# Optimization experiments

Hardware: AMD Instinct MI355X
Metric: run time of the kernel (lower is better)

## Reference

```python
import jax, jax.numpy as jnp
import numpy as np

H = 1024        # hidden_dim
NH = 8          # num_heads
HD = H // NH    # head_dim
EPS = 1e-5


def setup_inputs() -> dict:
    key = jax.random.key(0)
    ks = jax.random.split(key, 16)
    s = 0.02
    d = {
        'x': jax.random.normal(ks[0], (2, 2048, H), dtype=jnp.float32),
        'ln1_g': jnp.ones((H,), jnp.float32), 'ln1_b': jnp.zeros((H,), jnp.float32),
        'ln2_g': jnp.ones((H,), jnp.float32), 'ln2_b': jnp.zeros((H,), jnp.float32),
        'Wq': jax.random.normal(ks[1], (H, H), jnp.float32) * s,
        'bq': jnp.zeros((H,), jnp.float32),
        'Wk': jax.random.normal(ks[2], (H, H), jnp.float32) * s,
        'bk': jnp.zeros((H,), jnp.float32),
        'Wv': jax.random.normal(ks[3], (H, H), jnp.float32) * s,
        'bv': jnp.zeros((H,), jnp.float32),
        'Wo': jax.random.normal(ks[4], (H, H), jnp.float32) * s,
        'bo': jnp.zeros((H,), jnp.float32),
        'W1': jax.random.normal(ks[5], (H, 4 * H), jnp.float32) * s,
        'b1': jnp.zeros((4 * H,), jnp.float32),
        'W2': jax.random.normal(ks[6], (4 * H, H), jnp.float32) * s,
        'b2': jnp.zeros((H,), jnp.float32),
    }
    return d


def _layernorm(x, g, b):
    mu = jnp.mean(x, axis=-1, keepdims=True)
    var = jnp.mean(jnp.square(x - mu), axis=-1, keepdims=True)
    return (x - mu) * jax.lax.rsqrt(var + EPS) * g + b


def _block(x, ln1_g, ln1_b, ln2_g, ln2_b, Wq, bq, Wk, bk, Wv, bv, Wo, bo, W1, b1, W2, b2):
    B, S, _ = x.shape
    h = _layernorm(x, ln1_g, ln1_b)
    q = (h @ Wq + bq).reshape(B, S, NH, HD).transpose(0, 2, 1, 3)  # [B,NH,S,HD]
    k = (h @ Wk + bk).reshape(B, S, NH, HD).transpose(0, 2, 1, 3)
    v = (h @ Wv + bv).reshape(B, S, NH, HD).transpose(0, 2, 1, 3)
    scores = jnp.einsum('bhqd,bhkd->bhqk', q, k) / np.sqrt(HD)
    causal = jnp.tril(jnp.ones((S, S), bool))
    scores = jnp.where(causal, scores, -jnp.inf)
    attn = jax.nn.softmax(scores, axis=-1)
    y = jnp.einsum('bhqk,bhkd->bhqd', attn, v).transpose(0, 2, 1, 3).reshape(B, S, H)
    x = x + y @ Wo + bo
    h2 = _layernorm(x, ln2_g, ln2_b)
    m = jax.nn.gelu(h2 @ W1 + b1, approximate=False) @ W2 + b2
    return x + m


def reference(x, ln1_g, ln1_b, ln2_g, ln2_b, Wq, bq, Wk, bk, Wv, bv, Wo, bo, W1, b1, W2, b2):
    return _block(x, ln1_g, ln1_b, ln2_g, ln2_b, Wq, bq, Wk, bk, Wv, bv, Wo, bo, W1, b1, W2, b2)
```

## Files before the change

kernel.cpp:

```cpp
#include <hip/hip_runtime.h>
#include <hip/hip_bf16.h>
#include <math.h>

using bf16 = __hip_bfloat16;
typedef __attribute__((ext_vector_type(8))) short short8v;
typedef __attribute__((ext_vector_type(4))) float f32x4;
typedef __attribute__((ext_vector_type(16))) float f32x16;

#define DEV __device__ __forceinline__

DEV void load_lds16(const bf16* gsrc, bf16* ldst) {
  __builtin_amdgcn_global_load_lds((const __attribute__((address_space(1))) void*)gsrc,
                                   (__attribute__((address_space(3))) void*)ldst, 16, 0, 0);
}

DEV void swz8(int& bx, int& by, int gx, int gy) {
  const int n = gx * gy, c = n >> 3;
  int lin = bx + gx * by;
  lin = (lin & 7) * c + (lin >> 3);
  bx = lin % gx; by = lin / gx;
}

DEV unsigned pack2bf(float a, float b) {
  bf16 ba = __float2bfloat16(a), bb = __float2bfloat16(b);
  return (unsigned)*(unsigned short*)&ba | ((unsigned)*(unsigned short*)&bb << 16);
}

__global__ __launch_bounds__(256) void prep_kernel(
    const float* __restrict__ Wq, const float* __restrict__ Wk, const float* __restrict__ Wv,
    const float* __restrict__ Wo, const float* __restrict__ W1, const float* __restrict__ W2,
    bf16* __restrict__ WqT, bf16* __restrict__ WkT, bf16* __restrict__ WvT,
    bf16* __restrict__ WoT, bf16* __restrict__ W1T, bf16* __restrict__ W2T,
    const float* __restrict__ x, const float* __restrict__ ln1g, const float* __restrict__ ln1b,
    bf16* __restrict__ h) {
  __shared__ float tile[64][65];
  const int b = blockIdx.x;
  if (b >= 3072) {
    const int row = b - 3072, t = threadIdx.x;
    const float4 v = ((const float4*)(x + (size_t)row * 1024))[t];
    float s = v.x + v.y + v.z + v.w;
#pragma unroll
    for (int mm = 1; mm < 64; mm <<= 1) s += __shfl_xor(s, mm);
    __shared__ float r1[4], r2[4];
    if ((t & 63) == 0) r1[t >> 6] = s;
    __syncthreads();
    const float mean = (r1[0] + r1[1] + r1[2] + r1[3]) * (1.0f / 1024.0f);
    const float d0 = v.x - mean, d1 = v.y - mean, d2 = v.z - mean, d3 = v.w - mean;
    float s2 = d0 * d0 + d1 * d1 + d2 * d2 + d3 * d3;
#pragma unroll
    for (int mm = 1; mm < 64; mm <<= 1) s2 += __shfl_xor(s2, mm);
    if ((t & 63) == 0) r2[t >> 6] = s2;
    __syncthreads();
    const float var = (r2[0] + r2[1] + r2[2] + r2[3]) * (1.0f / 1024.0f);
    const float rinv = rsqrtf(var + 1e-5f);
    const int c = t * 4;
    bf16* o = h + (size_t)row * 1024 + c;
    o[0] = __float2bfloat16(d0 * rinv * ln1g[c + 0] + ln1b[c + 0]);
    o[1] = __float2bfloat16(d1 * rinv * ln1g[c + 1] + ln1b[c + 1]);
    o[2] = __float2bfloat16(d2 * rinv * ln1g[c + 2] + ln1b[c + 2]);
    o[3] = __float2bfloat16(d3 * rinv * ln1g[c + 3] + ln1b[c + 3]);
    return;
  }
  const float* W; bf16* WT; int K, N, n0, k0;
  if (b < 1024) {
    const int which = b >> 8, t = b & 255;
    W  = (which == 0) ? Wq  : (which == 1) ? Wk  : (which == 2) ? Wv  : Wo;
    WT = (which == 0) ? WqT : (which == 1) ? WkT : (which == 2) ? WvT : WoT;
    K = 1024; N = 1024; n0 = (t & 15) * 64; k0 = (t >> 4) * 64;
  } else if (b < 2048) {
    const int t = b - 1024;
    W = W1; WT = W1T; K = 1024; N = 4096; n0 = (t & 63) * 64; k0 = (t >> 6) * 64;
  } else {
    const int t = b - 2048;
    W = W2; WT = W2T; K = 4096; N = 1024; n0 = (t & 15) * 64; k0 = (t >> 4) * 64;
  }
  const int tx = threadIdx.x & 15, ty = threadIdx.x >> 4;
#pragma unroll
  for (int p = 0; p < 4; ++p) {
    int r = p * 16 + ty;
    float4 vv = *(const float4*)&W[(size_t)(k0 + r) * N + n0 + tx * 4];
    tile[r][tx * 4 + 0] = vv.x; tile[r][tx * 4 + 1] = vv.y;
    tile[r][tx * 4 + 2] = vv.z; tile[r][tx * 4 + 3] = vv.w;
  }
  __syncthreads();
#pragma unroll
  for (int p = 0; p < 4; ++p) {
    int n = p * 16 + ty;
    bf16* dst = WT + (size_t)(n0 + n) * K + k0 + tx * 4;
#pragma unroll
    for (int j = 0; j < 4; ++j) dst[j] = __float2bfloat16(tile[tx * 4 + j][n]);
  }
}

__global__ __launch_bounds__(256) void ln_kernel(const float* __restrict__ x,
                                                 const float* __restrict__ g,
                                                 const float* __restrict__ b,
                                                 bf16* __restrict__ out) {
  const int row = blockIdx.x, t = threadIdx.x;
  const float4 v = ((const float4*)(x + (size_t)row * 1024))[t];
  float s = v.x + v.y + v.z + v.w;
#pragma unroll
  for (int mm = 1; mm < 64; mm <<= 1) s += __shfl_xor(s, mm);
  __shared__ float r1[4], r2[4];
  if ((t & 63) == 0) r1[t >> 6] = s;
  __syncthreads();
  const float mean = (r1[0] + r1[1] + r1[2] + r1[3]) * (1.0f / 1024.0f);
  const float d0 = v.x - mean, d1 = v.y - mean, d2 = v.z - mean, d3 = v.w - mean;
  float s2 = d0 * d0 + d1 * d1 + d2 * d2 + d3 * d3;
#pragma unroll
  for (int mm = 1; mm < 64; mm <<= 1) s2 += __shfl_xor(s2, mm);
  if ((t & 63) == 0) r2[t >> 6] = s2;
  __syncthreads();
  const float var = (r2[0] + r2[1] + r2[2] + r2[3]) * (1.0f / 1024.0f);
  const float rinv = rsqrtf(var + 1e-5f);
  const int c = t * 4;
  bf16* o = out + (size_t)row * 1024 + c;
  o[0] = __float2bfloat16(d0 * rinv * g[c + 0] + b[c + 0]);
  o[1] = __float2bfloat16(d1 * rinv * g[c + 1] + b[c + 1]);
  o[2] = __float2bfloat16(d2 * rinv * g[c + 2] + b[c + 2]);
  o[3] = __float2bfloat16(d3 * rinv * g[c + 3] + b[c + 3]);
}

template <int EPI>
__global__ __launch_bounds__(512, 2) void gemm256(
    const bf16* __restrict__ A, const bf16* __restrict__ BT,
    const float* __restrict__ bias0, const float* __restrict__ bias1, const float* __restrict__ bias2,
    void* __restrict__ outp, int M, int N, int K) {
  __shared__ bf16 As[4][256 * 32];
  __shared__ bf16 Bs[4][256 * 32];
  const int tid = threadIdx.x;
  const int w = tid >> 6, l = tid & 63;
  const int wm = w >> 2, wn = w & 3;
  const int c = l & 15, h4 = l >> 4;
  int bx = blockIdx.x, by = blockIdx.y;
  swz8(bx, by, gridDim.x, gridDim.y);
  const int m0 = by * 256, n0 = bx * 256;

  const float* bias;
  int zz = 0;
  if (EPI == 0) {
    zz = n0 >> 10;
    bias = ((zz == 0) ? bias0 : (zz == 1) ? bias1 : bias2) - (zz << 10);
  } else {
    bias = bias0;
  }

  const int rl = l >> 2;
  const int ch = (l & 3) * 8;
  const int nkt = K >> 5;

  f32x4 acc[8][4] = {};

  auto STAGE_A = [&](int t, int b) {
    const bf16* src = A + (size_t)(m0 + rl) * K + t * 32 + ch;
    load_lds16(src + (size_t)((w * 2 + 0) * 16) * K, &As[b][(w * 2 + 0) * 512]);
    load_lds16(src + (size_t)((w * 2 + 1) * 16) * K, &As[b][(w * 2 + 1) * 512]);
  };
  auto STAGE_B = [&](int t, int b) {
    const bf16* src = BT + (size_t)(n0 + rl) * K + t * 32 + ch;
    load_lds16(src + (size_t)((w * 2 + 0) * 16) * K, &Bs[b][(w * 2 + 0) * 512]);
    load_lds16(src + (size_t)((w * 2 + 1) * 16) * K, &Bs[b][(w * 2 + 1) * 512]);
  };

  STAGE_A(0, 0); STAGE_B(0, 0);
  STAGE_A(1, 1); STAGE_B(1, 1);
  STAGE_A(2, 2); STAGE_B(2, 2);
  asm volatile("s_waitcnt vmcnt(8)" ::: "memory");
  __builtin_amdgcn_sched_barrier(0);
  __builtin_amdgcn_s_barrier();

  for (int t = 0; t < nkt; ++t) {
    const bf16* Ab = &As[t & 3][0];
    const bf16* Bb = &Bs[t & 3][0];
    short8v a[4], b[4];
#pragma unroll
    for (int i = 0; i < 4; ++i)
      a[i] = *(const short8v*)&Ab[(wm * 128 + i * 16 + c) * 32 + h4 * 8];
#pragma unroll
    for (int i = 0; i < 4; ++i)
      b[i] = *(const short8v*)&Bb[(wn * 64 + i * 16 + c) * 32 + h4 * 8];
    if (t + 3 < nkt) STAGE_A(t + 3, (t + 3) & 3);
    asm volatile("s_waitcnt lgkmcnt(0)" ::: "memory");
    __builtin_amdgcn_sched_barrier(0);
    __builtin_amdgcn_s_setprio(1);
#pragma unroll
    for (int mi = 0; mi < 4; ++mi)
#pragma unroll
      for (int ni = 0; ni < 4; ++ni)
        acc[mi][ni] = __builtin_amdgcn_mfma_f32_16x16x32_bf16(a[mi], b[ni], acc[mi][ni], 0, 0, 0);
    __builtin_amdgcn_s_setprio(0);
#pragma unroll
    for (int i = 0; i < 4; ++i)
      a[i] = *(const short8v*)&Ab[(wm * 128 + 64 + i * 16 + c) * 32 + h4 * 8];
    if (t + 3 < nkt) STAGE_B(t + 3, (t + 3) & 3);
    asm volatile("s_waitcnt lgkmcnt(0)" ::: "memory");
    __builtin_amdgcn_sched_barrier(0);
    __builtin_amdgcn_s_setprio(1);
#pragma unroll
    for (int mi = 0; mi < 4; ++mi)
#pragma unroll
      for (int ni = 0; ni < 4; ++ni)
        acc[4 + mi][ni] = __builtin_amdgcn_mfma_f32_16x16x32_bf16(a[mi], b[ni], acc[4 + mi][ni], 0, 0, 0);
    __builtin_amdgcn_s_setprio(0);
    if (t < nkt - 3)       asm volatile("s_waitcnt vmcnt(8)" ::: "memory");
    else if (t == nkt - 3) asm volatile("s_waitcnt vmcnt(4)" ::: "memory");
    else                   asm volatile("s_waitcnt vmcnt(0)" ::: "memory");
    __builtin_amdgcn_sched_barrier(0);
    __builtin_amdgcn_s_barrier();
  }

#pragma unroll
  for (int mi = 0; mi < 8; ++mi) {
#pragma unroll
    for (int ni = 0; ni < 4; ++ni) {
#pragma unroll
      for (int r = 0; r < 4; ++r) {
        const int m = m0 + wm * 128 + mi * 16 + h4 * 4 + r;
        const int n = n0 + wn * 64 + ni * 16 + c;
        float vv = acc[mi][ni][r] + bias[n];
        if (EPI == 0) {
          if (zz == 0) vv *= 0.08838834764831845f;
          const int bb = m >> 11, ss = m & 2047;
          const int n1 = n - (zz << 10);
          const int hh = n1 >> 7, dd = n1 & 127;
          ((bf16*)outp)[(size_t)zz * 4194304 + (((size_t)bb * 8 + hh) * 2048 + ss) * 128 + dd] =
              __float2bfloat16(vv);
        } else {
          const size_t idx = (size_t)m * N + n;
          const float u = 0.7978845608028654f * (vv + 0.044715f * vv * vv * vv);
          const float tt = __expf(2.0f * u);
          const float th = 1.0f - 2.0f / (tt + 1.0f);
          ((bf16*)outp)[idx] = __float2bfloat16(0.5f * vv * (1.0f + th));
        }
      }
    }
  }
}

template <int EPI, int MI>
__global__ __launch_bounds__(256) void gemm128(
    const bf16* __restrict__ A, const bf16* __restrict__ BT,
    const float* __restrict__ bias0, const float* __restrict__ bias1, const float* __restrict__ bias2,
    const float* __restrict__ res, void* __restrict__ outp,
    int M, int N, int K) {
  __shared__ bf16 As[2][MI * 1024];
  __shared__ bf16 Bs[2][128 * 32];
  const int tid = threadIdx.x;
  const int w = tid >> 6, l = tid & 63;
  const int wr = w >> 1, wc = w & 1;
  const int col = l & 15, hi = l >> 4;
  int bx = blockIdx.x, by = blockIdx.y;
  swz8(bx, by, gridDim.x, gridDim.y);
  const int m0 = by * (32 * MI), n0 = bx * 128;

  const float* bias = bias0;

  const int srow = l >> 2;
  const int scol = ((l & 3) ^ ((l >> 4) & 3)) * 8;
  const int rs = col * 4 + (hi ^ ((l >> 2) & 3));
  f32x4 acc[MI][4] = {};

  const int nk = K >> 5;
#pragma unroll
  for (int j = 0; j < MI / 2; ++j) {
    const int grp = w * (MI / 2) + j;
    load_lds16(A + (size_t)(m0 + grp * 16 + srow) * K + scol, &As[0][grp * 512]);
  }
#pragma unroll
  for (int j = 0; j < 2; ++j) {
    const int grp = w * 2 + j;
    load_lds16(BT + (size_t)(n0 + grp * 16 + srow) * K + scol, &Bs[0][grp * 512]);
  }
  __syncthreads();

  int cur = 0;
  for (int kt = 0; kt < nk; ++kt) {
    if (kt + 1 < nk) {
      const int k0n = (kt + 1) * 32;
#pragma unroll
      for (int j = 0; j < MI / 2; ++j) {
        const int grp = w * (MI / 2) + j;
        load_lds16(A + (size_t)(m0 + grp * 16 + srow) * K + k0n + scol, &As[cur ^ 1][grp * 512]);
      }
#pragma unroll
      for (int j = 0; j < 2; ++j) {
        const int grp = w * 2 + j;
        load_lds16(BT + (size_t)(n0 + grp * 16 + srow) * K + k0n + scol, &Bs[cur ^ 1][grp * 512]);
      }
    }
    __builtin_amdgcn_sched_barrier(0);

    short8v af[MI], bfr[4];
#pragma unroll
    for (int i = 0; i < MI; ++i)
      af[i] = *(const short8v*)&As[cur][(wr * MI + i) * 512 + rs * 8];
#pragma unroll
    for (int i = 0; i < 4; ++i)
      bfr[i] = *(const short8v*)&Bs[cur][(wc * 4 + i) * 512 + rs * 8];
#pragma unroll
    for (int mi = 0; mi < MI; ++mi)
#pragma unroll
      for (int ni = 0; ni < 4; ++ni)
        acc[mi][ni] = __builtin_amdgcn_mfma_f32_16x16x32_bf16(af[mi], bfr[ni], acc[mi][ni], 0, 0, 0);
    __syncthreads();
    cur ^= 1;
  }

#pragma unroll
  for (int mi = 0; mi < MI; ++mi) {
#pragma unroll
    for (int ni = 0; ni < 4; ++ni) {
#pragma unroll
      for (int r = 0; r < 4; ++r) {
        const int m = m0 + wr * (16 * MI) + mi * 16 + hi * 4 + r;
        const int n = n0 + wc * 64 + ni * 16 + col;
        const float vv = acc[mi][ni][r] + bias[n];
        const size_t idx = (size_t)m * N + n;
        ((float*)outp)[idx] = res[idx] + vv;
      }
    }
  }
}

__global__ __launch_bounds__(512, 1) void gemm_sk2(
    const bf16* __restrict__ A, const bf16* __restrict__ BT,
    const float* __restrict__ bias, const float* __restrict__ res, float* __restrict__ outp,
    int M, int N, int K) {
  __shared__ __align__(16) char lds_raw[131072];
  const int tid = threadIdx.x;
  const int w = tid >> 6, l = tid & 63;
  const int grp = w >> 2, wg = w & 3;
  const int wr = wg >> 1, wc = wg & 1;
  const int col = l & 15, hi = l >> 4;
  int bx = blockIdx.x, by = blockIdx.y;
  swz8(bx, by, gridDim.x, gridDim.y);
  const int m0 = by * 128, n0 = bx * 128;

  const int rl = l >> 2;
  const int ch = (l & 3) * 8;
  f32x4 acc[4][4] = {};

  const int KH = K >> 1;
  const int kbase = grp * KH;
  const int nkt = KH >> 5;

  auto ABUF = [&](int b) { return (bf16*)(lds_raw + grp * 65536 + b * 16384); };
  auto BBUF = [&](int b) { return (bf16*)(lds_raw + grp * 65536 + b * 16384 + 8192); };

  auto STAGE = [&](int t, int b) {
    const bf16* srcA = A + (size_t)(m0 + rl) * K + kbase + t * 32 + ch;
    const bf16* srcB = BT + (size_t)(n0 + rl) * K + kbase + t * 32 + ch;
    bf16* Ab = ABUF(b); bf16* Bb = BBUF(b);
    load_lds16(srcA + (size_t)((wg * 2 + 0) * 16) * K, Ab + (wg * 2 + 0) * 512);
    load_lds16(srcA + (size_t)((wg * 2 + 1) * 16) * K, Ab + (wg * 2 + 1) * 512);
    load_lds16(srcB + (size_t)((wg * 2 + 0) * 16) * K, Bb + (wg * 2 + 0) * 512);
    load_lds16(srcB + (size_t)((wg * 2 + 1) * 16) * K, Bb + (wg * 2 + 1) * 512);
  };

  STAGE(0, 0); STAGE(1, 1); STAGE(2, 2);
  asm volatile("s_waitcnt vmcnt(8)" ::: "memory");
  __builtin_amdgcn_sched_barrier(0);
  __builtin_amdgcn_s_barrier();

  for (int t = 0; t < nkt; ++t) {
    const bf16* Ab = ABUF(t & 3);
    const bf16* Bb = BBUF(t & 3);
    short8v af[4], bf_[4];
#pragma unroll
    for (int i = 0; i < 4; ++i) {
      af[i]  = *(const short8v*)&Ab[(wr * 64 + i * 16 + col) * 32 + hi * 8];
      bf_[i] = *(const short8v*)&Bb[(wc * 64 + i * 16 + col) * 32 + hi * 8];
    }
    if (t + 3 < nkt) STAGE(t + 3, (t + 3) & 3);
    asm volatile("s_waitcnt lgkmcnt(0)" ::: "memory");
    __builtin_amdgcn_sched_barrier(0);
    __builtin_amdgcn_s_setprio(1);
#pragma unroll
    for (int mi = 0; mi < 4; ++mi)
#pragma unroll
      for (int ni = 0; ni < 4; ++ni)
        acc[mi][ni] = __builtin_amdgcn_mfma_f32_16x16x32_bf16(af[mi], bf_[ni], acc[mi][ni], 0, 0, 0);
    __builtin_amdgcn_s_setprio(0);
    if (t < nkt - 3)       asm volatile("s_waitcnt vmcnt(8)" ::: "memory");
    else if (t == nkt - 3) asm volatile("s_waitcnt vmcnt(4)" ::: "memory");
    else                   asm volatile("s_waitcnt vmcnt(0)" ::: "memory");
    __builtin_amdgcn_sched_barrier(0);
    __builtin_amdgcn_s_barrier();
  }

  float* dump = (float*)lds_raw;
  if (grp == 1) {
#pragma unroll
    for (int mi = 0; mi < 4; ++mi)
#pragma unroll
      for (int ni = 0; ni < 4; ++ni)
#pragma unroll
        for (int r = 0; r < 4; ++r)
          dump[(wr * 64 + mi * 16 + hi * 4 + r) * 130 + wc * 64 + ni * 16 + col] = acc[mi][ni][r];
  }
  __syncthreads();
  if (grp == 0) {
#pragma unroll
    for (int mi = 0; mi < 4; ++mi) {
#pragma unroll
      for (int ni = 0; ni < 4; ++ni) {
#pragma unroll
        for (int r = 0; r < 4; ++r) {
          const int lrow = wr * 64 + mi * 16 + hi * 4 + r;
          const int lcol = wc * 64 + ni * 16 + col;
          const int m = m0 + lrow, n = n0 + lcol;
          const size_t idx = (size_t)m * N + n;
          outp[idx] = res[idx] + acc[mi][ni][r] + dump[lrow * 130 + lcol] + bias[n];
        }
      }
    }
  }
}

__global__ __launch_bounds__(512) void attn_kernel(const bf16* __restrict__ q,
                                                   const bf16* __restrict__ k,
                                                   const bf16* __restrict__ v,
                                                   bf16* __restrict__ y) {
  __shared__ __align__(16) char lds_raw[159744];
  int p = blockIdx.x, bh = blockIdx.y;
  swz8(p, bh, 16, 16);
  const int tid = threadIdx.x;
  const int w = tid >> 6, l = tid & 63;
  const int grp = w >> 2;
  const int wg  = w & 3;
  const int qs  = (w >> 1) & 1;
  const int ks  = w & 1;
  const int lq  = l & 31;
  const int lh  = l >> 5;

  const bf16* kbase = k + (size_t)bh * 2048 * 128;
  const bf16* vbase = v + (size_t)bh * 2048 * 128;
  const int bb = bh >> 3, hh = bh & 7;

  bf16* Psw = (bf16*)(lds_raw + 139264 + (size_t)w * 2560);

  const int klr = (l >> 4);
  const int kblk0 = l & 15;
  const int vr = (l & 31) * 2;
  const int vcb = (wg * 2 + (l >> 5)) * 16;

  for (int half = 0; half < 2; ++half) {
    const int qt = half ? p : (31 - p);
    const int q0 = qt * 64;
    const int T = qt + 1;
    const int n0 = (T + 1) >> 1;
    const int myn = grp ? (T >> 1) : n0;
    const int tb = grp ? n0 : 0;

    short8v qf[8];
    const bf16* qp = q + ((size_t)bh * 2048 + q0 + qs * 32 + lq) * 128 + lh * 8;
#pragma unroll
    for (int c = 0; c < 8; ++c) qf[c] = *(const short8v*)(qp + c * 16);

    f32x16 o[4] = {};
    float mx = -1e20f, sm = 0.f;

    if (myn > 0) {
      bf16* Ks0 = (bf16*)(lds_raw + (size_t)(grp * 2 + 0) * 16384);
      bf16* Vt0 = (bf16*)(lds_raw + 65536 + (size_t)(grp * 2 + 0) * 18432);
#pragma unroll
      for (int j = 0; j < 4; ++j) {
        const int lr = j * 4 + klr;
        const int blk = kblk0 ^ (lr & 7);
        load_lds16(kbase + (size_t)(tb * 64 + wg * 16 + lr) * 128 + blk * 8,
                   Ks0 + wg * 2048 + j * 512);
      }
      const bf16* vsrc = vbase + (size_t)(tb * 64 + vr) * 128 + vcb;
      short8v v00 = *(const short8v*)vsrc;
      short8v v01 = *(const short8v*)(vsrc + 8);
      short8v v10 = *(const short8v*)(vsrc + 128);
      short8v v11 = *(const short8v*)(vsrc + 136);
#pragma unroll
      for (int i = 0; i < 8; ++i) {
        *(unsigned int*)&Vt0[(vcb + i) * 72 + vr] =
            ((unsigned int)(unsigned short)v00[i]) | (((unsigned int)(unsigned short)v10[i]) << 16);
        *(unsigned int*)&Vt0[(vcb + 8 + i) * 72 + vr] =
            ((unsigned int)(unsigned short)v01[i]) | (((unsigned int)(unsigned short)v11[i]) << 16);
      }
    }
    __syncthreads();

    for (int it = 0; it < n0; ++it) {
      const int cur = it & 1;
      const bool active = it < myn;
      const bool havenext = (it + 1) < myn;
      bf16* KsCur = (bf16*)(lds_raw + (size_t)(grp * 2 + cur) * 16384);
      bf16* KsNxt = (bf16*)(lds_raw + (size_t)(grp * 2 + (cur ^ 1)) * 16384);
      bf16* VtCur = (bf16*)(lds_raw + 65536 + (size_t)(grp * 2 + cur) * 18432);
      bf16* VtNxt = (bf16*)(lds_raw + 65536 + (size_t)(grp * 2 + (cur ^ 1)) * 18432);

      short8v v00, v01, v10, v11;
      if (havenext) {
        const int nt = tb + it + 1;
#pragma unroll
        for (int j = 0; j < 4; ++j) {
          const int lr = j * 4 + klr;
          const int blk = kblk0 ^ (lr & 7);
          load_lds16(kbase + (size_t)(nt * 64 + wg * 16 + lr) * 128 + blk * 8,
                     KsNxt + wg * 2048 + j * 512);
        }
        const bf16* vsrc = vbase + (size_t)(nt * 64 + vr) * 128 + vcb;
        v00 = *(const short8v*)vsrc;
        v01 = *(const short8v*)(vsrc + 8);
        v10 = *(const short8v*)(vsrc + 128);
        v11 = *(const short8v*)(vsrc + 136);
      }

      if (active) {
        const int ktile = tb + it;
        f32x16 s = {};
        const int kr = ks * 32 + lq;
        const int swz = kr & 7;
        __builtin_amdgcn_s_setprio(1);
#pragma unroll
        for (int c = 0; c < 8; ++c) {
          const int gneed = 2 * c + lh;
          short8v kf = *(const short8v*)&KsCur[kr * 128 + ((gneed ^ swz) << 3)];
          s = __builtin_amdgcn_mfma_f32_32x32x16_bf16(kf, qf[c], s, 0, 0, 0);
        }
        __builtin_amdgcn_s_setprio(0);

        if (ktile == qt) {
          const int qloc = qs * 32 + lq;
#pragma unroll
          for (int reg = 0; reg < 16; ++reg) {
            const int kloc = ks * 32 + (reg & 3) + 8 * (reg >> 2) + 4 * lh;
            if (kloc > qloc) s[reg] = -1e30f;
          }
        }
        float t0 = fmaxf(fmaxf(s[0], s[1]), fmaxf(s[2], s[3]));
        float t1 = fmaxf(fmaxf(s[4], s[5]), fmaxf(s[6], s[7]));
        float t2 = fmaxf(fmaxf(s[8], s[9]), fmaxf(s[10], s[11]));
        float t3 = fmaxf(fmaxf(s[12], s[13]), fmaxf(s[14], s[15]));
        float t = fmaxf(fmaxf(t0, t1), fmaxf(t2, t3));
        t = fmaxf(t, __shfl_xor(t, 32));
        float mn;
        if (__all(t <= mx + 8.0f)) {
          mn = mx;
        } else {
          mn = fmaxf(mx, t);
          const float aa = __expf(mx - mn);
          sm *= aa;
#pragma unroll
          for (int db = 0; db < 4; ++db) o[db] *= aa;
          mx = mn;
        }
        float ps = 0.f;
        unsigned u[8];
#pragma unroll
        for (int rq = 0; rq < 4; ++rq) {
          const float p0 = __expf(s[rq * 4 + 0] - mn);
          const float p1 = __expf(s[rq * 4 + 1] - mn);
          const float p2 = __expf(s[rq * 4 + 2] - mn);
          const float p3 = __expf(s[rq * 4 + 3] - mn);
          ps += (p0 + p1) + (p2 + p3);
          u[rq * 2 + 0] = pack2bf(p0, p1);
          u[rq * 2 + 1] = pack2bf(p2, p3);
        }
        sm += ps;
#pragma unroll
        for (int rq = 0; rq < 4; ++rq) {
          uint2 pk; pk.x = u[rq * 2]; pk.y = u[rq * 2 + 1];
          *(uint2*)&Psw[lq * 40 + rq * 8 + lh * 4] = pk;
        }
      }

      if (havenext) {
#pragma unroll
        for (int i = 0; i < 8; ++i) {
          *(unsigned int*)&VtNxt[(vcb + i) * 72 + vr] =
              ((unsigned int)(unsigned short)v00[i]) | (((unsigned int)(unsigned short)v10[i]) << 16);
          *(unsigned int*)&VtNxt[(vcb + 8 + i) * 72 + vr] =
              ((unsigned int)(unsigned short)v01[i]) | (((unsigned int)(unsigned short)v11[i]) << 16);
        }
      }

      if (active) {
        asm volatile("s_waitcnt lgkmcnt(0)" ::: "memory");
        __builtin_amdgcn_s_setprio(1);
#pragma unroll
        for (int kc = 0; kc < 2; ++kc) {
          short8v pf = *(const short8v*)&Psw[lq * 40 + kc * 16 + lh * 8];
#pragma unroll
          for (int db = 0; db < 4; ++db) {
            short8v vf = *(const short8v*)&VtCur[(db * 32 + lq) * 72 + ks * 32 + kc * 16 + lh * 8];
            o[db] = __builtin_amdgcn_mfma_f32_32x32x16_bf16(vf, pf, o[db], 0, 0, 0);
          }
        }
        __builtin_amdgcn_s_setprio(0);
      }
      __syncthreads();
    }

    sm += __shfl_xor(sm, 32);

    float* smmx = (float*)(lds_raw + 139264);
    if (l < 32) { smmx[w * 64 + l] = sm; smmx[w * 64 + 32 + l] = mx; }
    const bool merger = (grp == 0 && ks == 0);
    if (!merger) {
      const int slot = qs * 3 + (grp * 2 + ks - 1);
      float* dst = (float*)(lds_raw + slot * 17408);
#pragma unroll
      for (int db = 0; db < 4; ++db) {
#pragma unroll
        for (int rq = 0; rq < 4; ++rq) {
          f32x4 vv;
          vv[0] = o[db][rq * 4 + 0]; vv[1] = o[db][rq * 4 + 1];
          vv[2] = o[db][rq * 4 + 2]; vv[3] = o[db][rq * 4 + 3];
          *(f32x4*)&dst[lq * 132 + db * 32 + rq * 8 + lh * 4] = vv;
        }
      }
    }
    __syncthreads();
    if (merger) {
      const int w01 = w + 1, w10 = 4 + qs * 2, w11 = 5 + qs * 2;
      const float sm01 = smmx[w01 * 64 + lq], mx01 = smmx[w01 * 64 + 32 + lq];
      const float sm10 = smmx[w10 * 64 + lq], mx10 = smmx[w10 * 64 + 32 + lq];
      const float sm11 = smmx[w11 * 64 + lq], mx11 = smmx[w11 * 64 + 32 + lq];
      const float M = fmaxf(fmaxf(mx, mx01), fmaxf(mx10, mx11));
      const float a00 = __expf(mx - M), a01 = __expf(mx01 - M);
      const float a10 = __expf(mx10 - M), a11 = __expf(mx11 - M);
      const float inv = 1.0f / (sm * a00 + sm01 * a01 + sm10 * a10 + sm11 * a11);
      const float* d01 = (const float*)(lds_raw + (qs * 3 + 0) * 17408);
      const float* d10 = (const float*)(lds_raw + (qs * 3 + 1) * 17408);
      const float* d11 = (const float*)(lds_raw + (qs * 3 + 2) * 17408);
      const int qg = q0 + qs * 32 + lq;
      bf16* yrow = y + ((size_t)bb * 2048 + qg) * 1024 + hh * 128;
#pragma unroll
      for (int db = 0; db < 4; ++db) {
#pragma unroll
        for (int rq = 0; rq < 4; ++rq) {
          const int off = lq * 132 + db * 32 + rq * 8 + lh * 4;
          const f32x4 v01 = *(const f32x4*)&d01[off];
          const f32x4 v10 = *(const f32x4*)&d10[off];
          const f32x4 v11 = *(const f32x4*)&d11[off];
          const float r0 = (o[db][rq * 4 + 0] * a00 + v01[0] * a01 + v10[0] * a10 + v11[0] * a11) * inv;
          const float r1 = (o[db][rq * 4 + 1] * a00 + v01[1] * a01 + v10[1] * a10 + v11[1] * a11) * inv;
          const float r2 = (o[db][rq * 4 + 2] * a00 + v01[2] * a01 + v10[2] * a10 + v11[2] * a11) * inv;
          const float r3 = (o[db][rq * 4 + 3] * a00 + v01[3] * a01 + v10[3] * a10 + v11[3] * a11) * inv;
          uint2 pk; pk.x = pack2bf(r0, r1); pk.y = pack2bf(r2, r3);
          *(uint2*)(yrow + db * 32 + rq * 8 + lh * 4) = pk;
        }
      }
    }
    __syncthreads();
  }
}

extern "C" void kernel_launch(void* const* d_in, const int* in_sizes, int n_in,
                              void* d_out, int out_size, void* d_ws, size_t ws_size,
                              hipStream_t stream) {
  const float* x    = (const float*)d_in[0];
  const float* ln1g = (const float*)d_in[1];
  const float* ln1b = (const float*)d_in[2];
  const float* ln2g = (const float*)d_in[3];
  const float* ln2b = (const float*)d_in[4];
  const float* Wq   = (const float*)d_in[5];
  const float* bq   = (const float*)d_in[6];
  const float* Wk   = (const float*)d_in[7];
  const float* bk   = (const float*)d_in[8];
  const float* Wv   = (const float*)d_in[9];
  const float* bv   = (const float*)d_in[10];
  const float* Wo   = (const float*)d_in[11];
  const float* bo   = (const float*)d_in[12];
  const float* W1   = (const float*)d_in[13];
  const float* b1   = (const float*)d_in[14];
  const float* W2   = (const float*)d_in[15];
  const float* b2   = (const float*)d_in[16];
  float* out = (float*)d_out;
  char* ws = (char*)d_ws;
  const size_t MB = 1024 * 1024;

  bf16* WqT = (bf16*)(ws + 0 * MB);
  bf16* WkT = (bf16*)(ws + 2 * MB);
  bf16* WvT = (bf16*)(ws + 4 * MB);
  bf16* WoT = (bf16*)(ws + 6 * MB);
  bf16* W1T = (bf16*)(ws + 8 * MB);
  bf16* W2T = (bf16*)(ws + 16 * MB);
  bf16* h   = (bf16*)(ws + 24 * MB);
  bf16* qb  = (bf16*)(ws + 32 * MB);
  bf16* kb  = (bf16*)(ws + 40 * MB);
  bf16* vb  = (bf16*)(ws + 48 * MB);
  bf16* y   = (bf16*)(ws + 56 * MB);
  bf16* g   = (bf16*)(ws + 32 * MB);
  float* x1 = (float*)(ws + 64 * MB);
  bf16* h2  = h;

  prep_kernel<<<7168, 256, 0, stream>>>(Wq, Wk, Wv, Wo, W1, W2, WqT, WkT, WvT, WoT, W1T, W2T,
                                        x, ln1g, ln1b, h);

  gemm256<0><<<dim3(12, 16), 512, 0, stream>>>(h, WqT, bq, bk, bv, qb, 4096, 3072, 1024);

  attn_kernel<<<dim3(16, 16), 512, 0, stream>>>(qb, kb, vb, y);

  gemm128<1, 2><<<dim3(8, 64), 256, 0, stream>>>(y, WoT, bo, nullptr, nullptr, x, x1,
                                                 4096, 1024, 1024);

  ln_kernel<<<4096, 256, 0, stream>>>(x1, ln2g, ln2b, h2);

  gemm256<2><<<dim3(16, 16), 512, 0, stream>>>(h2, W1T, b1, nullptr, nullptr, g,
                                               4096, 4096, 1024);

  gemm_sk2<<<dim3(8, 32), 512, 0, stream>>>(g, W2T, b2, x1, out, 4096, 1024, 4096);
}
```

Measured before the change: 227.1 us.

## Split QK MFMA chain, make softmax rescale unconditional, reuse split-K GEMM for Wo

The attention QK^T accumulation is split into two independent MFMA accumulator chains that are summed afterwards, shortening the dependent MFMA chain. The online softmax drops the lazy-rescale branch with its wave vote and always rescales o and sm, and the causal mask becomes a predicated loop instead of a branch. The output projection GEMM now uses the existing split-K 512-thread kernel in place of the 128-tile kernel, whose code is removed. Trade-offs: more accumulator registers, unconditional exp and multiplies per tile, and a different tiling for the Wo GEMM.

```diff
diff --git a/kernel.cpp b/kernel.cpp
--- a/kernel.cpp
+++ b/kernel.cpp
@@ -237,91 +237,6 @@
   }
 }
 
-template <int EPI, int MI>
-__global__ __launch_bounds__(256) void gemm128(
-    const bf16* __restrict__ A, const bf16* __restrict__ BT,
-    const float* __restrict__ bias0, const float* __restrict__ bias1, const float* __restrict__ bias2,
-    const float* __restrict__ res, void* __restrict__ outp,
-    int M, int N, int K) {
-  __shared__ bf16 As[2][MI * 1024];
-  __shared__ bf16 Bs[2][128 * 32];
-  const int tid = threadIdx.x;
-  const int w = tid >> 6, l = tid & 63;
-  const int wr = w >> 1, wc = w & 1;
-  const int col = l & 15, hi = l >> 4;
-  int bx = blockIdx.x, by = blockIdx.y;
-  swz8(bx, by, gridDim.x, gridDim.y);
-  const int m0 = by * (32 * MI), n0 = bx * 128;
-
-  const float* bias = bias0;
-
-  const int srow = l >> 2;
-  const int scol = ((l & 3) ^ ((l >> 4) & 3)) * 8;
-  const int rs = col * 4 + (hi ^ ((l >> 2) & 3));
-  f32x4 acc[MI][4] = {};
-
-  const int nk = K >> 5;
-#pragma unroll
-  for (int j = 0; j < MI / 2; ++j) {
-    const int grp = w * (MI / 2) + j;
-    load_lds16(A + (size_t)(m0 + grp * 16 + srow) * K + scol, &As[0][grp * 512]);
-  }
-#pragma unroll
-  for (int j = 0; j < 2; ++j) {
-    const int grp = w * 2 + j;
-    load_lds16(BT + (size_t)(n0 + grp * 16 + srow) * K + scol, &Bs[0][grp * 512]);
-  }
-  __syncthreads();
-
-  int cur = 0;
-  for (int kt = 0; kt < nk; ++kt) {
-    if (kt + 1 < nk) {
-      const int k0n = (kt + 1) * 32;
-#pragma unroll
-      for (int j = 0; j < MI / 2; ++j) {
-        const int grp = w * (MI / 2) + j;
-        load_lds16(A + (size_t)(m0 + grp * 16 + srow) * K + k0n + scol, &As[cur ^ 1][grp * 512]);
-      }
-#pragma unroll
-      for (int j = 0; j < 2; ++j) {
-        const int grp = w * 2 + j;
-        load_lds16(BT + (size_t)(n0 + grp * 16 + srow) * K + k0n + scol, &Bs[cur ^ 1][grp * 512]);
-      }
-    }
-    __builtin_amdgcn_sched_barrier(0);
-
-    short8v af[MI], bfr[4];
-#pragma unroll
-    for (int i = 0; i < MI; ++i)
-      af[i] = *(const short8v*)&As[cur][(wr * MI + i) * 512 + rs * 8];
-#pragma unroll
-    for (int i = 0; i < 4; ++i)
-      bfr[i] = *(const short8v*)&Bs[cur][(wc * 4 + i) * 512 + rs * 8];
-#pragma unroll
-    for (int mi = 0; mi < MI; ++mi)
-#pragma unroll
-      for (int ni = 0; ni < 4; ++ni)
-        acc[mi][ni] = __builtin_amdgcn_mfma_f32_16x16x32_bf16(af[mi], bfr[ni], acc[mi][ni], 0, 0, 0);
-    __syncthreads();
-    cur ^= 1;
-  }
-
-#pragma unroll
-  for (int mi = 0; mi < MI; ++mi) {
-#pragma unroll
-    for (int ni = 0; ni < 4; ++ni) {
-#pragma unroll
-      for (int r = 0; r < 4; ++r) {
-        const int m = m0 + wr * (16 * MI) + mi * 16 + hi * 4 + r;
-        const int n = n0 + wc * 64 + ni * 16 + col;
-        const float vv = acc[mi][ni][r] + bias[n];
-        const size_t idx = (size_t)m * N + n;
-        ((float*)outp)[idx] = res[idx] + vv;
-      }
-    }
-  }
-}
-
 __global__ __launch_bounds__(512, 1) void gemm_sk2(
     const bf16* __restrict__ A, const bf16* __restrict__ BT,
     const float* __restrict__ bias, const float* __restrict__ res, float* __restrict__ outp,
@@ -513,25 +428,26 @@
 
       if (active) {
         const int ktile = tb + it;
-        f32x16 s = {};
+        f32x16 s_lo = {}, s_hi = {};
         const int kr = ks * 32 + lq;
         const int swz = kr & 7;
         __builtin_amdgcn_s_setprio(1);
 #pragma unroll
-        for (int c = 0; c < 8; ++c) {
-          const int gneed = 2 * c + lh;
-          short8v kf = *(const short8v*)&KsCur[kr * 128 + ((gneed ^ swz) << 3)];
-          s = __builtin_amdgcn_mfma_f32_32x32x16_bf16(kf, qf[c], s, 0, 0, 0);
+        for (int c = 0; c < 4; ++c) {
+          short8v kf0 = *(const short8v*)&KsCur[kr * 128 + (((2 * c + lh) ^ swz) << 3)];
+          short8v kf1 = *(const short8v*)&KsCur[kr * 128 + (((2 * (c + 4) + lh) ^ swz) << 3)];
+          s_lo = __builtin_amdgcn_mfma_f32_32x32x16_bf16(kf0, qf[c], s_lo, 0, 0, 0);
+          s_hi = __builtin_amdgcn_mfma_f32_32x32x16_bf16(kf1, qf[c + 4], s_hi, 0, 0, 0);
         }
         __builtin_amdgcn_s_setprio(0);
-
-        if (ktile == qt) {
-          const int qloc = qs * 32 + lq;
-#pragma unroll
-          for (int reg = 0; reg < 16; ++reg) {
-            const int kloc = ks * 32 + (reg & 3) + 8 * (reg >> 2) + 4 * lh;
-            if (kloc > qloc) s[reg] = -1e30f;
-          }
+        f32x16 s = s_lo + s_hi;
+
+        const bool diag = (ktile == qt);
+        const int qloc = qs * 32 + lq;
+#pragma unroll
+        for (int reg = 0; reg < 16; ++reg) {
+          const int kloc = ks * 32 + (reg & 3) + 8 * (reg >> 2) + 4 * lh;
+          if (diag && (kloc > qloc)) s[reg] = -1e30f;
         }
         float t0 = fmaxf(fmaxf(s[0], s[1]), fmaxf(s[2], s[3]));
         float t1 = fmaxf(fmaxf(s[4], s[5]), fmaxf(s[6], s[7]));
@@ -539,17 +455,8 @@
         float t3 = fmaxf(fmaxf(s[12], s[13]), fmaxf(s[14], s[15]));
         float t = fmaxf(fmaxf(t0, t1), fmaxf(t2, t3));
         t = fmaxf(t, __shfl_xor(t, 32));
-        float mn;
-        if (__all(t <= mx + 8.0f)) {
-          mn = mx;
-        } else {
-          mn = fmaxf(mx, t);
-          const float aa = __expf(mx - mn);
-          sm *= aa;
-#pragma unroll
-          for (int db = 0; db < 4; ++db) o[db] *= aa;
-          mx = mn;
-        }
+        const float mn = fmaxf(mx, t);
+        const float aa = __expf(mx - mn);
         float ps = 0.f;
         unsigned u[8];
 #pragma unroll
@@ -562,12 +469,15 @@
           u[rq * 2 + 0] = pack2bf(p0, p1);
           u[rq * 2 + 1] = pack2bf(p2, p3);
         }
-        sm += ps;
+        sm = sm * aa + ps;
+        mx = mn;
 #pragma unroll
         for (int rq = 0; rq < 4; ++rq) {
           uint2 pk; pk.x = u[rq * 2]; pk.y = u[rq * 2 + 1];
           *(uint2*)&Psw[lq * 40 + rq * 8 + lh * 4] = pk;
         }
+#pragma unroll
+        for (int db = 0; db < 4; ++db) o[db] *= aa;
       }
 
       if (havenext) {
@@ -698,8 +608,7 @@
 
   attn_kernel<<<dim3(16, 16), 512, 0, stream>>>(qb, kb, vb, y);
 
-  gemm128<1, 2><<<dim3(8, 64), 256, 0, stream>>>(y, WoT, bo, nullptr, nullptr, x, x1,
-                                                 4096, 1024, 1024);
+  gemm_sk2<<<dim3(8, 32), 512, 0, stream>>>(y, WoT, bo, x, x1, 4096, 1024, 1024);
 
   ln_kernel<<<4096, 256, 0, stream>>>(x1, ln2g, ln2b, h2);
 
```

Result: no change. 225.7 us (-0.6%).
